# Performance work log

Measured on AMD Instinct MI355X. Metric: run time of the kernel, lower is better.

## Reference

```python
import jax, jax.numpy as jnp
import numpy as np

N_NODES = 100000
N_EDGES = 1600000
IN_F = 128
OUT_F = 64
LN_EPS = 1e-5


def setup_inputs() -> dict:
    key = jax.random.key(0)
    ks = jax.random.split(key, 8)
    stdv = 1.0 / np.sqrt(OUT_F)
    x = jax.random.normal(ks[0], (N_NODES, IN_F), dtype=jnp.float32)
    weight = jax.random.uniform(ks[1], (IN_F, OUT_F), minval=-stdv, maxval=stdv, dtype=jnp.float32)
    bias = jnp.zeros((OUT_F,), dtype=jnp.float32)
    ln_gamma = jnp.ones((OUT_F,), dtype=jnp.float32)
    ln_beta = jnp.zeros((OUT_F,), dtype=jnp.float32)
    # residual nn.Linear(in_features, out_features): weight [out, in], bias [out]
    bound = 1.0 / np.sqrt(IN_F)
    res_w = jax.random.uniform(ks[2], (OUT_F, IN_F), minval=-bound, maxval=bound, dtype=jnp.float32)
    res_b = jax.random.uniform(ks[3], (OUT_F,), minval=-bound, maxval=bound, dtype=jnp.float32)
    edge_src = jax.random.randint(ks[4], (N_EDGES,), 0, N_NODES, dtype=jnp.int64 if jax.config.jax_enable_x64 else jnp.int32)
    edge_dst = jax.random.randint(ks[5], (N_EDGES,), 0, N_NODES, dtype=jnp.int64 if jax.config.jax_enable_x64 else jnp.int32)
    edge_weight = jax.random.uniform(ks[6], (N_EDGES,), dtype=jnp.float32)
    return {
        "x": x, "weight": weight, "bias": bias,
        "ln_gamma": ln_gamma, "ln_beta": ln_beta,
        "res_w": res_w, "res_b": res_b,
        "edge_weight": edge_weight, "edge_src": edge_src, "edge_dst": edge_dst,
    }


def reference(x, weight, bias, ln_gamma, ln_beta, res_w, res_b, edge_weight, edge_src, edge_dst):
    # support = x @ W                                   [N, OUT_F]
    support = x @ weight
    # spmm: out[d] = sum_{e: dst(e)=d} w_e * support[src(e)]
    msg = support[edge_src] * edge_weight[:, None]      # [E, OUT_F]
    out = jax.ops.segment_sum(msg, edge_dst, num_segments=x.shape[0])
    # bias
    out = out + bias
    # layernorm over feature dim
    mu = jnp.mean(out, axis=-1, keepdims=True)
    var = jnp.var(out, axis=-1, keepdims=True)
    out = (out - mu) * jax.lax.rsqrt(var + LN_EPS) * ln_gamma + ln_beta
    # relu activation
    out = jax.nn.relu(out)
    # residual linear on the input
    out = out + x @ res_w.T + res_b
    return out
```

## Files before the change

### kernel.cpp

```cpp
#include <hip/hip_runtime.h>

#define N_NODES 100000
#define N_EDGES 1600000
#define IN_F 128
#define OUT_F 64
#define LN_EPS 1e-5f

#define BSHIFT 6
#define BNODES 64
#define NB ((N_NODES + BNODES - 1) >> BSHIFT)

#define CAP 2048
#define CH 2048

#define MT 64
#define NGEMM ((N_NODES + MT - 1) / MT)
#define LDA 136

#define K1_BLOCKS 1792
#define K1_GEMM_BLOCKS 768
#define K1_PART_BLOCKS 1024
#define K1_THREADS 256
#define K1_PART_CHUNK ((N_EDGES + K1_PART_BLOCKS - 1) / K1_PART_BLOCKS)

typedef __attribute__((ext_vector_type(8))) short short8;
typedef __attribute__((ext_vector_type(4))) float f32x4;

__device__ __forceinline__ unsigned short f2bf(float f) {
  unsigned int u = __float_as_uint(f);
  unsigned int r = (u + 0x7FFFu + ((u >> 16) & 1u)) >> 16;
  return (unsigned short)r;
}
__device__ __forceinline__ float bf2f(unsigned short h) {
  return __uint_as_float((unsigned int)h << 16);
}

__global__ __launch_bounds__(K1_THREADS) void gemm_partition(
    const float* __restrict__ x, const float* __restrict__ W,
    const float* __restrict__ res_w, const float* __restrict__ res_b,
    const int* __restrict__ esrc, const int* __restrict__ edst,
    const float* __restrict__ ew, unsigned short* __restrict__ support,
    float* __restrict__ resid, int* __restrict__ gcount,
    int2* __restrict__ part) {
  __shared__ __align__(16) char smem[34816];
  const int tid = threadIdx.x;
  const int bid = blockIdx.x;
  const int role = bid % 7;

  if (role < 3) {
    const int gb = (bid / 7) * 3 + role;
    short* bt = (short*)smem;

    for (int i = tid; i < 128 * 64; i += K1_THREADS) {
      const int k = i >> 6, n = i & 63;
      bt[n * LDA + k] = (short)f2bf(W[i]);
    }
    for (int i = tid; i < 64 * 128; i += K1_THREADS) {
      const int np = i >> 7, k = i & 127;
      bt[(64 + np) * LDA + k] = (short)f2bf(res_w[i]);
    }
    __syncthreads();

    const int w = tid >> 6;
    const int lane = tid & 63;
    const int m16 = lane & 15;
    const int quad = lane >> 4;

    float rbv[8];
#pragma unroll
    for (int nt = 0; nt < 8; ++nt)
      rbv[nt] = (nt >= 4) ? res_b[nt * 16 + m16 - 64] : 0.f;

    const float4* xr = (const float4*)x;

    for (int g = gb; g < NGEMM; g += K1_GEMM_BLOCKS) {
      const size_t row0 = (size_t)g * MT;
      const size_t arow = row0 + (size_t)(w * 16 + m16);
      const bool ok = arow < N_NODES;
      const size_t abase = arow * 32 + quad * 2;

      short8 afr[4];
#pragma unroll
      for (int kt = 0; kt < 4; ++kt) {
        float4 u = make_float4(0.f, 0.f, 0.f, 0.f);
        float4 v = make_float4(0.f, 0.f, 0.f, 0.f);
        if (ok) {
          u = xr[abase + kt * 8];
          v = xr[abase + kt * 8 + 1];
        }
        short8 a;
        a[0] = (short)f2bf(u.x); a[1] = (short)f2bf(u.y);
        a[2] = (short)f2bf(u.z); a[3] = (short)f2bf(u.w);
        a[4] = (short)f2bf(v.x); a[5] = (short)f2bf(v.y);
        a[6] = (short)f2bf(v.z); a[7] = (short)f2bf(v.w);
        afr[kt] = a;
      }

#pragma unroll
      for (int nt = 0; nt < 8; ++nt) {
        f32x4 acc = {0.f, 0.f, 0.f, 0.f};
#pragma unroll
        for (int kt = 0; kt < 4; ++kt) {
          const short8 bfr =
              *(const short8*)(&bt[(nt * 16 + m16) * LDA + kt * 32 + quad * 8]);
          acc = __builtin_amdgcn_mfma_f32_16x16x32_bf16(afr[kt], bfr, acc, 0, 0, 0);
        }
        const int col = nt * 16 + m16;
#pragma unroll
        for (int r = 0; r < 4; ++r) {
          const size_t row = row0 + w * 16 + quad * 4 + r;
          if (row < N_NODES) {
            if (col < 64) support[row * OUT_F + col] = f2bf(acc[r]);
            else          resid[row * OUT_F + (col - 64)] = acc[r] + rbv[nt];
          }
        }
      }
    }
  } else {
    const int pb = (bid / 7) * 4 + (role - 3);
    int*   ssrc = (int*)smem;
    int*   sdst = (int*)(smem + 6256);
    float* sew  = (float*)(smem + 12512);
    int*   lcnt = (int*)(smem + 18768);
    int*   lpos = (int*)(smem + 25024);
    for (int i = tid; i < NB; i += K1_THREADS) lcnt[i] = 0;
    __syncthreads();
    const int beg = pb * K1_PART_CHUNK;
    const int end = min(beg + K1_PART_CHUNK, N_EDGES);
    const int n = end - beg;
    for (int i = tid; i < n; i += K1_THREADS) {
      const int d = edst[beg + i];
      ssrc[i] = esrc[beg + i];
      sdst[i] = d;
      sew[i] = ew[beg + i];
      atomicAdd(&lcnt[d >> BSHIFT], 1);
    }
    __syncthreads();
    for (int i = tid; i < NB; i += K1_THREADS)
      lpos[i] = lcnt[i] ? atomicAdd(&gcount[i], lcnt[i]) : 0;
    __syncthreads();
    for (int i = tid; i < n; i += K1_THREADS) {
      const int d = sdst[i];
      const int b = d >> BSHIFT;
      const int p = atomicAdd(&lpos[b], 1);
      part[(size_t)b * CAP + p] =
          make_int2((ssrc[i] << BSHIFT) | (d & 63), __float_as_int(sew[i]));
    }
  }
}

__global__ __launch_bounds__(512, 4) void bucket_sort_accum(
    const unsigned short* __restrict__ support, const int2* __restrict__ part,
    const int* __restrict__ gcount, const float* __restrict__ resid,
    const float* __restrict__ bias, const float* __restrict__ gamma,
    const float* __restrict__ beta, float* __restrict__ out) {
  __shared__ int2 estage[CH];
  __shared__ int2 esorted[CH];
  __shared__ int bcnt2[BNODES];
  __shared__ int bseg[BNODES];
  __shared__ int bpos[BNODES];
  const int tid = threadIdx.x;
  const int o = tid & 63;
  const int wid = tid >> 6;
  const int b = blockIdx.x;
  const int cnt = min(gcount[b], CAP);
  const size_t beg = (size_t)b * CAP;
  const size_t end = beg + cnt;

  float acc8[8];
#pragma unroll
  for (int t = 0; t < 8; ++t) acc8[t] = 0.f;

  for (size_t base = beg; base < end; base += CH) {
    const int n = (int)min((size_t)CH, end - base);
    __syncthreads();
    if (tid < BNODES) bcnt2[tid] = 0;
    __syncthreads();

    for (int i = tid; i < n; i += 512) {
      const int2 r = part[base + i];
      estage[i] = r;
      atomicAdd(&bcnt2[r.x & 63], 1);
    }
    __syncthreads();

    if (wid == 0) {
      const int v = bcnt2[o];
      int incl = v;
#pragma unroll
      for (int off = 1; off < 64; off <<= 1) {
        const int u = __shfl_up(incl, off, 64);
        if (o >= off) incl += u;
      }
      bseg[o] = incl - v;
      bpos[o] = incl - v;
    }
    __syncthreads();

    for (int i = tid; i < n; i += 512) {
      const int2 r = estage[i];
      const int p = atomicAdd(&bpos[r.x & 63], 1);
      esorted[p] = r;
    }
    __syncthreads();

#pragma unroll
    for (int t = 0; t < 8; ++t) {
      const int j = wid * 8 + t;
      const int s = bseg[j];
      const int c = bcnt2[j];
      float a = acc8[t];
      int e = 0;
      for (; e + 4 <= c; e += 4) {
        const int2 m0 = esorted[s + e + 0];
        const int2 m1 = esorted[s + e + 1];
        const int2 m2 = esorted[s + e + 2];
        const int2 m3 = esorted[s + e + 3];
        const float v0 = bf2f(support[((size_t)((unsigned)m0.x >> 6) << 6) + o]);
        const float v1 = bf2f(support[((size_t)((unsigned)m1.x >> 6) << 6) + o]);
        const float v2 = bf2f(support[((size_t)((unsigned)m2.x >> 6) << 6) + o]);
        const float v3 = bf2f(support[((size_t)((unsigned)m3.x >> 6) << 6) + o]);
        a = fmaf(v0, __int_as_float(m0.y), a);
        a = fmaf(v1, __int_as_float(m1.y), a);
        a = fmaf(v2, __int_as_float(m2.y), a);
        a = fmaf(v3, __int_as_float(m3.y), a);
      }
      for (; e < c; ++e) {
        const int2 m = esorted[s + e];
        a = fmaf(bf2f(support[((size_t)((unsigned)m.x >> 6) << 6) + o]),
                 __int_as_float(m.y), a);
      }
      acc8[t] = a;
    }
  }

  const float bi = bias[o];
  const float ga = gamma[o];
  const float be = beta[o];
#pragma unroll
  for (int t = 0; t < 8; ++t) {
    const int j = wid * 8 + t;
    const int nid = (b << BSHIFT) + j;
    if (nid < N_NODES) {
      const float v = acc8[t] + bi;
      float s = v, sq = v * v;
#pragma unroll
      for (int off = 32; off > 0; off >>= 1) {
        s += __shfl_xor(s, off, 64);
        sq += __shfl_xor(sq, off, 64);
      }
      const float mu = s * (1.f / 64.f);
      const float var = sq * (1.f / 64.f) - mu * mu;
      const float r = rsqrtf(var + LN_EPS);
      const float nrm = fmaxf((v - mu) * r * ga + be, 0.f);
      out[(size_t)nid * OUT_F + o] = nrm + resid[(size_t)nid * OUT_F + o];
    }
  }
}

extern "C" void kernel_launch(void* const* d_in, const int* in_sizes, int n_in,
                              void* d_out, int out_size, void* d_ws,
                              size_t ws_size, hipStream_t stream) {
  const float* x      = (const float*)d_in[0];
  const float* weight = (const float*)d_in[1];
  const float* bias   = (const float*)d_in[2];
  const float* gamma  = (const float*)d_in[3];
  const float* beta   = (const float*)d_in[4];
  const float* res_w  = (const float*)d_in[5];
  const float* res_b  = (const float*)d_in[6];
  const float* ew     = (const float*)d_in[7];
  const int*   esrc   = (const int*)d_in[8];
  const int*   edst   = (const int*)d_in[9];
  float* out = (float*)d_out;

  char* ws = (char*)d_ws;
  size_t off = 0;
  auto alloc = [&](size_t bytes) {
    void* p = ws + off;
    off += (bytes + 255) & ~(size_t)255;
    return p;
  };
  unsigned short* support = (unsigned short*)alloc((size_t)N_NODES * OUT_F * 2);
  float* resid   = (float*)alloc((size_t)N_NODES * OUT_F * sizeof(float));
  int2*  part    = (int2*)alloc((size_t)NB * CAP * sizeof(int2));
  int*   gcount  = (int*)alloc((size_t)NB * sizeof(int));

  hipMemsetAsync(gcount, 0, (size_t)NB * sizeof(int), stream);

  gemm_partition<<<K1_BLOCKS, K1_THREADS, 0, stream>>>(
      x, weight, res_w, res_b, esrc, edst, ew, support, resid, gcount, part);
  bucket_sort_accum<<<NB, 512, 0, stream>>>(support, part, gcount, resid,
                                            bias, gamma, beta, out);
}
```

Baseline: 210.1 us.

## Reshape K1 LDS layouts and rebalance grid for five-blocks-per-CU occupancy

Stores the bf16 weight tile in LDS in a k-chunk-major layout so MFMA B-fragment reads are contiguous per lane, removing the padded LDA layout. The partition path now packs each edge record once into an int2 and keeps a 16-bit bucket id, and reuses the count array as the position array. Together these cut shared memory to 32KB. The grid shrinks to 1280 blocks split 2:3 between GEMM and partition, with launch bounds asking for 5 blocks per CU. Larger per-block edge chunks and fewer GEMM blocks change the load balance and could lengthen the tail.

New measurement: 257.4 us. 1.22x slower.

```diff
diff --git a/kernel.cpp b/kernel.cpp
--- a/kernel.cpp
+++ b/kernel.cpp
@@ -15,13 +15,12 @@
 
 #define MT 64
 #define NGEMM ((N_NODES + MT - 1) / MT)
-#define LDA 136
-
-#define K1_BLOCKS 1792
-#define K1_GEMM_BLOCKS 768
-#define K1_PART_BLOCKS 1024
+
+#define K1_BLOCKS 1280
+#define K1_GEMM_BLOCKS 512
+#define K1_PART_BLOCKS 768
 #define K1_THREADS 256
-#define K1_PART_CHUNK ((N_EDGES + K1_PART_BLOCKS - 1) / K1_PART_BLOCKS)
+#define K1_PART_CHUNK 2084
 
 typedef __attribute__((ext_vector_type(8))) short short8;
 typedef __attribute__((ext_vector_type(4))) float f32x4;
@@ -35,29 +34,30 @@
   return __uint_as_float((unsigned int)h << 16);
 }
 
-__global__ __launch_bounds__(K1_THREADS) void gemm_partition(
+__global__ __launch_bounds__(K1_THREADS, 5) void gemm_partition(
     const float* __restrict__ x, const float* __restrict__ W,
     const float* __restrict__ res_w, const float* __restrict__ res_b,
     const int* __restrict__ esrc, const int* __restrict__ edst,
     const float* __restrict__ ew, unsigned short* __restrict__ support,
     float* __restrict__ resid, int* __restrict__ gcount,
     int2* __restrict__ part) {
-  __shared__ __align__(16) char smem[34816];
+  __shared__ __align__(16) char smem[32768];
   const int tid = threadIdx.x;
   const int bid = blockIdx.x;
-  const int role = bid % 7;
-
-  if (role < 3) {
-    const int gb = (bid / 7) * 3 + role;
-    short* bt = (short*)smem;
+  const int grp = bid / 5;
+  const int role = bid % 5;
+
+  if (role < 2) {
+    const int gb = grp * 2 + role;
+    short* bts = (short*)smem;
 
     for (int i = tid; i < 128 * 64; i += K1_THREADS) {
       const int k = i >> 6, n = i & 63;
-      bt[n * LDA + k] = (short)f2bf(W[i]);
+      bts[((k >> 3) << 10) + (n << 3) + (k & 7)] = (short)f2bf(W[i]);
     }
     for (int i = tid; i < 64 * 128; i += K1_THREADS) {
       const int np = i >> 7, k = i & 127;
-      bt[(64 + np) * LDA + k] = (short)f2bf(res_w[i]);
+      bts[((k >> 3) << 10) + ((64 + np) << 3) + (k & 7)] = (short)f2bf(res_w[i]);
     }
     __syncthreads();
 
@@ -72,6 +72,7 @@
       rbv[nt] = (nt >= 4) ? res_b[nt * 16 + m16 - 64] : 0.f;
 
     const float4* xr = (const float4*)x;
+    const short8* btp = (const short8*)smem;
 
     for (int g = gb; g < NGEMM; g += K1_GEMM_BLOCKS) {
       const size_t row0 = (size_t)g * MT;
@@ -101,8 +102,7 @@
         f32x4 acc = {0.f, 0.f, 0.f, 0.f};
 #pragma unroll
         for (int kt = 0; kt < 4; ++kt) {
-          const short8 bfr =
-              *(const short8*)(&bt[(nt * 16 + m16) * LDA + kt * 32 + quad * 8]);
+          const short8 bfr = btp[(((kt << 2) + quad) << 7) + (nt << 4) + m16];
           acc = __builtin_amdgcn_mfma_f32_16x16x32_bf16(afr[kt], bfr, acc, 0, 0, 0);
         }
         const int col = nt * 16 + m16;
@@ -117,12 +117,10 @@
       }
     }
   } else {
-    const int pb = (bid / 7) * 4 + (role - 3);
-    int*   ssrc = (int*)smem;
-    int*   sdst = (int*)(smem + 6256);
-    float* sew  = (float*)(smem + 12512);
-    int*   lcnt = (int*)(smem + 18768);
-    int*   lpos = (int*)(smem + 25024);
+    const int pb = grp * 3 + (role - 2);
+    int2*   rec = (int2*)smem;
+    unsigned short* sbk = (unsigned short*)(smem + 16672);
+    int*    lcnt = (int*)(smem + 20840);
     for (int i = tid; i < NB; i += K1_THREADS) lcnt[i] = 0;
     __syncthreads();
     const int beg = pb * K1_PART_CHUNK;
@@ -130,21 +128,22 @@
     const int n = end - beg;
     for (int i = tid; i < n; i += K1_THREADS) {
       const int d = edst[beg + i];
-      ssrc[i] = esrc[beg + i];
-      sdst[i] = d;
-      sew[i] = ew[beg + i];
-      atomicAdd(&lcnt[d >> BSHIFT], 1);
-    }
-    __syncthreads();
-    for (int i = tid; i < NB; i += K1_THREADS)
-      lpos[i] = lcnt[i] ? atomicAdd(&gcount[i], lcnt[i]) : 0;
+      const int s = esrc[beg + i];
+      rec[i] = make_int2((s << BSHIFT) | (d & 63), __float_as_int(ew[beg + i]));
+      const int b = d >> BSHIFT;
+      sbk[i] = (unsigned short)b;
+      atomicAdd(&lcnt[b], 1);
+    }
+    __syncthreads();
+    for (int i = tid; i < NB; i += K1_THREADS) {
+      const int c = lcnt[i];
+      lcnt[i] = c ? atomicAdd(&gcount[i], c) : 0;
+    }
     __syncthreads();
     for (int i = tid; i < n; i += K1_THREADS) {
-      const int d = sdst[i];
-      const int b = d >> BSHIFT;
-      const int p = atomicAdd(&lpos[b], 1);
-      part[(size_t)b * CAP + p] =
-          make_int2((ssrc[i] << BSHIFT) | (d & 63), __float_as_int(sew[i]));
+      const int b = sbk[i];
+      const int p = atomicAdd(&lcnt[b], 1);
+      part[(size_t)b * CAP + p] = rec[i];
     }
   }
 }
```
